# Kernel tuning notes

Measured on AMD Instinct MI355X. Metric: run time of the kernel, lower is better.

Reference implementation:

```python
import jax, jax.numpy as jnp
import numpy as np
from jax import lax

NUM_LAYERS = 3
NUM_QUBITS = 8
BATCH = 131072
DIM = 2 ** NUM_QUBITS  # 256


def _rot_mats(params):
    # params: (L, Q, 3) angles for RX, RY, RZ. Returns combined U = RZ @ RY @ RX, (L, Q, 2, 2) complex64.
    half = params * 0.5
    cx = jnp.cos(half[..., 0]).astype(jnp.complex64)
    sx = jnp.sin(half[..., 0]).astype(jnp.complex64)
    cy = jnp.cos(half[..., 1]).astype(jnp.complex64)
    sy = jnp.sin(half[..., 1]).astype(jnp.complex64)
    ezm = jnp.exp(-1j * half[..., 2]).astype(jnp.complex64)
    ezp = jnp.exp(1j * half[..., 2]).astype(jnp.complex64)
    zero = jnp.zeros_like(cx)
    RX = jnp.stack([jnp.stack([cx, -1j * sx], -1), jnp.stack([-1j * sx, cx], -1)], -2)
    RY = jnp.stack([jnp.stack([cy, -sy], -1), jnp.stack([sy, cy], -1)], -2)
    RZ = jnp.stack([jnp.stack([ezm, zero], -1), jnp.stack([zero, ezp], -1)], -2)
    return jnp.einsum('lqij,lqjk,lqkm->lqim', RZ, RY, RX)


def _apply_1q(state, U, wire):
    # state: (B, 2,2,...,2); wire w lives on axis w+1 (PennyLane wire 0 = most significant bit)
    ax = wire + 1
    return jnp.moveaxis(jnp.tensordot(U, state, axes=((1,), (ax,))), 0, ax)


def _apply_cnot(state, ctrl, tgt):
    c_ax, t_ax = ctrl + 1, tgt + 1
    s0 = lax.index_in_dim(state, 0, axis=c_ax, keepdims=True)
    s1 = lax.index_in_dim(state, 1, axis=c_ax, keepdims=True)
    s1 = jnp.flip(s1, axis=t_ax)
    return jnp.concatenate([s0, s1], axis=c_ax)


def _circuit(params, state_re, state_im):
    U = _rot_mats(params)  # (L, Q, 2, 2)
    state = (state_re + 1j * state_im).astype(jnp.complex64)
    state = state.reshape((state.shape[0],) + (2,) * NUM_QUBITS)
    for l in range(NUM_LAYERS):
        for q in range(NUM_QUBITS):
            state = _apply_1q(state, U[l, q], q)
        for q in range(NUM_QUBITS):
            state = _apply_cnot(state, q, (q + 1) % NUM_QUBITS)
    state = state.reshape(state.shape[0], DIM)
    # probability that wire 0 measures |0>: sum |amp|^2 over first half of amplitudes
    half = state[:, : DIM // 2]
    return jnp.sum(half.real ** 2 + half.imag ** 2, axis=1).astype(jnp.float32)


def setup_inputs() -> dict:
    key = jax.random.key(0)
    k1, k2, k3 = jax.random.split(key, 3)
    params = jax.random.uniform(k1, (NUM_LAYERS, NUM_QUBITS, 3), dtype=jnp.float32)
    sr = jax.random.normal(k2, (BATCH, DIM), dtype=jnp.float32)
    si = jax.random.normal(k3, (BATCH, DIM), dtype=jnp.float32)
    norm = jnp.sqrt(jnp.sum(sr ** 2 + si ** 2, axis=1, keepdims=True))
    return {"params": params, "state_re": sr / norm, "state_im": si / norm}


def reference(params, state_re, state_im):
    return _circuit(params, state_re, state_im)
```

## Files before the change

### kernel.cpp

```cpp
#include <hip/hip_runtime.h>
#include <stdint.h>

#define NLAYERS 3
#define NQ 8
#define DIM 256
#define KDIM 512
#define BM 64
#define NBLK (131072 / BM)

typedef float  f32x4  __attribute__((ext_vector_type(4)));
typedef __bf16 bf16x8 __attribute__((ext_vector_type(8)));

__device__ __forceinline__ unsigned short f2bf(float f){
    union { float f; uint32_t u; } v; v.f = f;
    uint32_t u = v.u;
    u += 0x7fffu + ((u >> 16) & 1u);
    return (unsigned short)(u >> 16);
}

__device__ __forceinline__ float2 cmul(float2 a, float2 b){
    return make_float2(a.x*b.x - a.y*b.y, a.x*b.y + a.y*b.x);
}

__device__ __forceinline__ void gload_lds16(void* lds, const void* g){
    __builtin_amdgcn_global_load_lds(
        (const __attribute__((address_space(1))) unsigned int*)g,
        (__attribute__((address_space(3))) unsigned int*)lds,
        16, 0, 0);
}

__global__ __launch_bounds__(256) void build_g_kernel(const float* __restrict__ params,
                                                      unsigned short* __restrict__ G){
    __shared__ float2 st[2][DIM];
    __shared__ float2 gm[NLAYERS*NQ][4];
    const int j = blockIdx.x;
    const int i = threadIdx.x;

    if (i < NLAYERS*NQ){
        const float* pp = params + i*3;
        float hx = 0.5f*pp[0], hy = 0.5f*pp[1], hz = 0.5f*pp[2];
        float cx = cosf(hx), sx = sinf(hx);
        float cy = cosf(hy), sy = sinf(hy);
        float cz = cosf(hz), sz = sinf(hz);
        float2 ezm = make_float2(cz, -sz), ezp = make_float2(cz, sz);
        float2 m00 = make_float2( cy*cx,  sy*sx);
        float2 m01 = make_float2(-sy*cx, -cy*sx);
        float2 m10 = make_float2( sy*cx, -cy*sx);
        float2 m11 = make_float2( cy*cx, -sy*sx);
        gm[i][0] = cmul(ezm, m00);
        gm[i][1] = cmul(ezm, m01);
        gm[i][2] = cmul(ezp, m10);
        gm[i][3] = cmul(ezp, m11);
    }

    int psrc = i;
    #pragma unroll
    for (int q = NQ-1; q >= 0; --q){
        int c  = 7 - q;
        int tb = 7 - ((q + 1) & 7);
        psrc = ((psrc >> c) & 1) ? (psrc ^ (1 << tb)) : psrc;
    }

    int cur = 0;
    st[0][i] = make_float2(i == j ? 1.0f : 0.0f, 0.0f);
    __syncthreads();

    for (int l = 0; l < NLAYERS; ++l){
        for (int q = 0; q < NQ; ++q){
            float2 U0a = gm[l*NQ+q][0], U0b = gm[l*NQ+q][1];
            float2 U1a = gm[l*NQ+q][2], U1b = gm[l*NQ+q][3];
            int p  = 7 - q;
            int bs = (i >> p) & 1;
            int i0 = i & ~(1 << p), i1 = i | (1 << p);
            float2 a0 = st[cur][i0], a1 = st[cur][i1];
            float2 ua = bs ? U1a : U0a;
            float2 ub = bs ? U1b : U0b;
            float2 r;
            r.x = ua.x*a0.x - ua.y*a0.y + ub.x*a1.x - ub.y*a1.y;
            r.y = ua.x*a0.y + ua.y*a0.x + ub.x*a1.y + ub.y*a1.x;
            st[cur ^ 1][i] = r;
            cur ^= 1;
            __syncthreads();
        }
        float2 r = st[cur][psrc];
        st[cur ^ 1][i] = r;
        cur ^= 1;
        __syncthreads();
    }

    const int m = i & 127;
    float2 a = st[cur][m];
    unsigned short lo, hi;
    if (i < 128){ lo = f2bf(a.x); hi = f2bf(-a.y); }
    else        { lo = f2bf(a.y); hi = f2bf( a.x); }
    G[(size_t)i*KDIM + j]        = lo;
    G[(size_t)i*KDIM + j + DIM]  = hi;
}

__global__ __launch_bounds__(256, 3) void qform_kernel(const float* __restrict__ sr,
                                                       const float* __restrict__ si,
                                                       const unsigned short* __restrict__ G,
                                                       float* __restrict__ out){
    __shared__ float          As[BM * 64];
    __shared__ unsigned short Bs[DIM * 64];
    __shared__ float red[4 * BM];

    const int tid  = threadIdx.x;
    const int lane = tid & 63;
    const int w    = tid >> 6;
    const int l15  = lane & 15;
    const int quad = lane >> 4;
    const int x7   = l15 & 7;
    const size_t mbase = (size_t)blockIdx.x * BM;

    f32x4 acc[4][4];
    const f32x4 vzero = {0.0f, 0.0f, 0.0f, 0.0f};
    #pragma unroll
    for (int ii = 0; ii < 4; ++ii)
        #pragma unroll
        for (int jj = 0; jj < 4; ++jj)
            acc[ii][jj] = vzero;

    for (int kc = 0; kc < 8; ++kc){
        __syncthreads();
        {
            const float* Zsrc = (kc < 4) ? sr : si;
            const int kcol = (kc & 3) * 64;
            #pragma unroll
            for (int i = 0; i < 4; ++i){
                const int c  = w*4 + i;
                const int ar = c*4 + (lane >> 4);
                const int gg = (lane & 15) ^ (ar & 7);
                const float* gp = Zsrc + (mbase + ar)*DIM + kcol + gg*4;
                gload_lds16(&As[c*256], gp);
            }
        }
        {
            #pragma unroll
            for (int i = 0; i < 8; ++i){
                const int c  = w*8 + i;
                const int rb = c*8 + (lane >> 3);
                const int gb = (lane & 7) ^ (rb & 7);
                const unsigned short* gp = G + (size_t)rb*KDIM + kc*64 + gb*8;
                gload_lds16(&Bs[c*512], gp);
            }
        }
        __syncthreads();

        #pragma unroll
        for (int ks = 0; ks < 2; ++ks){
            bf16x8 a[4], b[4];
            const int g0 = ks*8 + quad*2;
            #pragma unroll
            for (int ii = 0; ii < 4; ++ii){
                const int m = ii*16 + l15;
                union { float4 v; uint32_t u[4]; } h0, h1;
                h0.v = *(const float4*)&As[m*64 + ((g0    ) ^ x7)*4];
                h1.v = *(const float4*)&As[m*64 + ((g0 + 1) ^ x7)*4];
                union { uint32_t u[4]; bf16x8 f; } pk;
                pk.u[0] = __builtin_amdgcn_perm(h0.u[1], h0.u[0], 0x07060302);
                pk.u[1] = __builtin_amdgcn_perm(h0.u[3], h0.u[2], 0x07060302);
                pk.u[2] = __builtin_amdgcn_perm(h1.u[1], h1.u[0], 0x07060302);
                pk.u[3] = __builtin_amdgcn_perm(h1.u[3], h1.u[2], 0x07060302);
                a[ii] = pk.f;
            }
            const int gB = ks*4 + quad;
            #pragma unroll
            for (int jj = 0; jj < 4; ++jj){
                const int n = w*64 + jj*16 + l15;
                b[jj] = *(const bf16x8*)&Bs[n*64 + (gB ^ x7)*8];
            }
            #pragma unroll
            for (int ii = 0; ii < 4; ++ii)
                #pragma unroll
                for (int jj = 0; jj < 4; ++jj)
                    acc[ii][jj] = __builtin_amdgcn_mfma_f32_16x16x32_bf16(
                        a[ii], b[jj], acc[ii][jj], 0, 0, 0);
        }
    }

    float s[4][4];
    #pragma unroll
    for (int ii = 0; ii < 4; ++ii)
        #pragma unroll
        for (int r = 0; r < 4; ++r){
            float t = 0.0f;
            #pragma unroll
            for (int jj = 0; jj < 4; ++jj){ float v = acc[ii][jj][r]; t += v*v; }
            s[ii][r] = t;
        }
    #pragma unroll
    for (int ii = 0; ii < 4; ++ii)
        #pragma unroll
        for (int r = 0; r < 4; ++r){
            float t = s[ii][r];
            t += __shfl_xor(t, 1);
            t += __shfl_xor(t, 2);
            t += __shfl_xor(t, 4);
            t += __shfl_xor(t, 8);
            s[ii][r] = t;
        }
    if (l15 == 0){
        #pragma unroll
        for (int ii = 0; ii < 4; ++ii)
            #pragma unroll
            for (int r = 0; r < 4; ++r)
                red[w*64 + ii*16 + quad*4 + r] = s[ii][r];
    }
    __syncthreads();
    if (tid < 64){
        float o = red[tid] + red[64 + tid] + red[128 + tid] + red[192 + tid];
        out[mbase + tid] = o;
    }
}

extern "C" void kernel_launch(void* const* d_in, const int* in_sizes, int n_in,
                              void* d_out, int out_size, void* d_ws, size_t ws_size,
                              hipStream_t stream){
    const float* params = (const float*)d_in[0];
    const float* sr     = (const float*)d_in[1];
    const float* si     = (const float*)d_in[2];
    unsigned short* G   = (unsigned short*)d_ws;
    float* out          = (float*)d_out;

    build_g_kernel<<<dim3(DIM), dim3(256), 0, stream>>>(params, G);
    qform_kernel<<<dim3(NBLK), dim3(256), 0, stream>>>(sr, si, G, out);
}
```

Measured before the change: 289.3 us.

## Keep whole half-unitary in LDS and stream state rows directly into registers

Replaces the real-embedded 512x256 GEMM with a complex 256x128 product: the weight image (real and imaginary parts of the first half of the unitary) is loaded into LDS once per 1024-thread persistent block. State rows are then read straight from global into registers with one-step prefetch, using four MFMAs per complex tile. Only the wire-0 half of outputs is computed, which removes half the B-matrix work and avoids the per-k-chunk LDS staging and barriers. The costs are a 128KB LDS footprint that allows one block per CU, uncoalesced per-lane row loads, and serialized loops with unroll 1.

```diff
diff --git a/kernel.cpp b/kernel.cpp
--- a/kernel.cpp
+++ b/kernel.cpp
@@ -4,9 +4,8 @@
 #define NLAYERS 3
 #define NQ 8
 #define DIM 256
-#define KDIM 512
-#define BM 64
-#define NBLK (131072 / BM)
+#define HALF 128
+#define BATCH 131072
 
 typedef float  f32x4  __attribute__((ext_vector_type(4)));
 typedef __bf16 bf16x8 __attribute__((ext_vector_type(8)));
@@ -29,8 +28,8 @@
         16, 0, 0);
 }
 
-__global__ __launch_bounds__(256) void build_g_kernel(const float* __restrict__ params,
-                                                      unsigned short* __restrict__ G){
+__global__ __launch_bounds__(256) void build_w_kernel(const float* __restrict__ params,
+                                                      unsigned short* __restrict__ W){
     __shared__ float2 st[2][DIM];
     __shared__ float2 gm[NLAYERS*NQ][4];
     const int j = blockIdx.x;
@@ -90,127 +89,110 @@
 
     const int m = i & 127;
     float2 a = st[cur][m];
-    unsigned short lo, hi;
-    if (i < 128){ lo = f2bf(a.x); hi = f2bf(-a.y); }
-    else        { lo = f2bf(a.y); hi = f2bf( a.x); }
-    G[(size_t)i*KDIM + j]        = lo;
-    G[(size_t)i*KDIM + j + DIM]  = hi;
-}
-
-__global__ __launch_bounds__(256, 3) void qform_kernel(const float* __restrict__ sr,
-                                                       const float* __restrict__ si,
-                                                       const unsigned short* __restrict__ G,
-                                                       float* __restrict__ out){
-    __shared__ float          As[BM * 64];
-    __shared__ unsigned short Bs[DIM * 64];
-    __shared__ float red[4 * BM];
+    const uint32_t off = (uint32_t)m*256u
+                       + ((((uint32_t)j >> 3) ^ ((uint32_t)m & 7u)) << 3)
+                       + ((uint32_t)j & 7u);
+    if (i < 128) W[off]          = f2bf(a.x);
+    else         W[32768u + off] = f2bf(a.y);
+}
+
+__global__ __launch_bounds__(1024) void qform2_kernel(const float* __restrict__ sr,
+                                                      const float* __restrict__ si,
+                                                      const unsigned short* __restrict__ W,
+                                                      float* __restrict__ out){
+    __shared__ unsigned short Bs[65536];
 
     const int tid  = threadIdx.x;
     const int lane = tid & 63;
     const int w    = tid >> 6;
     const int l15  = lane & 15;
     const int quad = lane >> 4;
-    const int x7   = l15 & 7;
-    const size_t mbase = (size_t)blockIdx.x * BM;
-
-    f32x4 acc[4][4];
-    const f32x4 vzero = {0.0f, 0.0f, 0.0f, 0.0f};
+
     #pragma unroll
-    for (int ii = 0; ii < 4; ++ii)
+    for (int r = 0; r < 8; ++r){
+        const int c = w*8 + r;
+        gload_lds16(&Bs[c*512], W + (size_t)c*512 + lane*8);
+    }
+    __syncthreads();
+
+    const size_t row0 = (size_t)blockIdx.x * 512 + (size_t)w * 32;
+
+    #pragma unroll 1
+    for (int t = 0; t < 2; ++t){
+        const float* ar = sr + (row0 + (size_t)(t*16 + l15)) * DIM;
+        const float* ai = si + (row0 + (size_t)(t*16 + l15)) * DIM;
+
+        f32x4 accR[8], accI[8];
+        const f32x4 z = {0.0f, 0.0f, 0.0f, 0.0f};
         #pragma unroll
-        for (int jj = 0; jj < 4; ++jj)
-            acc[ii][jj] = vzero;
-
-    for (int kc = 0; kc < 8; ++kc){
-        __syncthreads();
-        {
-            const float* Zsrc = (kc < 4) ? sr : si;
-            const int kcol = (kc & 3) * 64;
+        for (int jf = 0; jf < 8; ++jf){ accR[jf] = z; accI[jf] = z; }
+
+        float4 r0 = *(const float4*)(ar + quad*8);
+        float4 r1 = *(const float4*)(ar + quad*8 + 4);
+        float4 q0 = *(const float4*)(ai + quad*8);
+        float4 q1 = *(const float4*)(ai + quad*8 + 4);
+
+        #pragma unroll 1
+        for (int ks = 0; ks < 8; ++ks){
+            union { float4 v; uint32_t u[4]; } ha, hb;
+            union { uint32_t u[4]; bf16x8 f; } pr, pi, pn;
+            ha.v = r0; hb.v = r1;
+            pr.u[0] = __builtin_amdgcn_perm(ha.u[1], ha.u[0], 0x07060302);
+            pr.u[1] = __builtin_amdgcn_perm(ha.u[3], ha.u[2], 0x07060302);
+            pr.u[2] = __builtin_amdgcn_perm(hb.u[1], hb.u[0], 0x07060302);
+            pr.u[3] = __builtin_amdgcn_perm(hb.u[3], hb.u[2], 0x07060302);
+            ha.v = q0; hb.v = q1;
+            pi.u[0] = __builtin_amdgcn_perm(ha.u[1], ha.u[0], 0x07060302);
+            pi.u[1] = __builtin_amdgcn_perm(ha.u[3], ha.u[2], 0x07060302);
+            pi.u[2] = __builtin_amdgcn_perm(hb.u[1], hb.u[0], 0x07060302);
+            pi.u[3] = __builtin_amdgcn_perm(hb.u[3], hb.u[2], 0x07060302);
+            pn.u[0] = pi.u[0] ^ 0x80008000u;
+            pn.u[1] = pi.u[1] ^ 0x80008000u;
+            pn.u[2] = pi.u[2] ^ 0x80008000u;
+            pn.u[3] = pi.u[3] ^ 0x80008000u;
+            const bf16x8 fr = pr.f;
+            const bf16x8 fi = pi.f;
+            const bf16x8 fn = pn.f;
+
+            const int nk = (ks < 7) ? (ks + 1) : 7;
+            r0 = *(const float4*)(ar + nk*32 + quad*8);
+            r1 = *(const float4*)(ar + nk*32 + quad*8 + 4);
+            q0 = *(const float4*)(ai + nk*32 + quad*8);
+            q1 = *(const float4*)(ai + nk*32 + quad*8 + 4);
+
+            const int ub = l15*256 + (((ks*4 + quad) ^ (l15 & 7)) << 3);
+
             #pragma unroll
-            for (int i = 0; i < 4; ++i){
-                const int c  = w*4 + i;
-                const int ar = c*4 + (lane >> 4);
-                const int gg = (lane & 15) ^ (ar & 7);
-                const float* gp = Zsrc + (mbase + ar)*DIM + kcol + gg*4;
-                gload_lds16(&As[c*256], gp);
+            for (int jf = 0; jf < 8; ++jf){
+                const bf16x8 br = *(const bf16x8*)&Bs[ub + jf*4096];
+                const bf16x8 bi = *(const bf16x8*)&Bs[32768 + ub + jf*4096];
+                accR[jf] = __builtin_amdgcn_mfma_f32_16x16x32_bf16(fr, br, accR[jf], 0, 0, 0);
+                accR[jf] = __builtin_amdgcn_mfma_f32_16x16x32_bf16(fn, bi, accR[jf], 0, 0, 0);
+                accI[jf] = __builtin_amdgcn_mfma_f32_16x16x32_bf16(fr, bi, accI[jf], 0, 0, 0);
+                accI[jf] = __builtin_amdgcn_mfma_f32_16x16x32_bf16(fi, br, accI[jf], 0, 0, 0);
             }
         }
-        {
-            #pragma unroll
-            for (int i = 0; i < 8; ++i){
-                const int c  = w*8 + i;
-                const int rb = c*8 + (lane >> 3);
-                const int gb = (lane & 7) ^ (rb & 7);
-                const unsigned short* gp = G + (size_t)rb*KDIM + kc*64 + gb*8;
-                gload_lds16(&Bs[c*512], gp);
-            }
-        }
-        __syncthreads();
-
-        #pragma unroll
-        for (int ks = 0; ks < 2; ++ks){
-            bf16x8 a[4], b[4];
-            const int g0 = ks*8 + quad*2;
-            #pragma unroll
-            for (int ii = 0; ii < 4; ++ii){
-                const int m = ii*16 + l15;
-                union { float4 v; uint32_t u[4]; } h0, h1;
-                h0.v = *(const float4*)&As[m*64 + ((g0    ) ^ x7)*4];
-                h1.v = *(const float4*)&As[m*64 + ((g0 + 1) ^ x7)*4];
-                union { uint32_t u[4]; bf16x8 f; } pk;
-                pk.u[0] = __builtin_amdgcn_perm(h0.u[1], h0.u[0], 0x07060302);
-                pk.u[1] = __builtin_amdgcn_perm(h0.u[3], h0.u[2], 0x07060302);
-                pk.u[2] = __builtin_amdgcn_perm(h1.u[1], h1.u[0], 0x07060302);
-                pk.u[3] = __builtin_amdgcn_perm(h1.u[3], h1.u[2], 0x07060302);
-                a[ii] = pk.f;
-            }
-            const int gB = ks*4 + quad;
-            #pragma unroll
-            for (int jj = 0; jj < 4; ++jj){
-                const int n = w*64 + jj*16 + l15;
-                b[jj] = *(const bf16x8*)&Bs[n*64 + (gB ^ x7)*8];
-            }
-            #pragma unroll
-            for (int ii = 0; ii < 4; ++ii)
-                #pragma unroll
-                for (int jj = 0; jj < 4; ++jj)
-                    acc[ii][jj] = __builtin_amdgcn_mfma_f32_16x16x32_bf16(
-                        a[ii], b[jj], acc[ii][jj], 0, 0, 0);
-        }
-    }
-
-    float s[4][4];
-    #pragma unroll
-    for (int ii = 0; ii < 4; ++ii)
+
+        float s[4];
         #pragma unroll
         for (int r = 0; r < 4; ++r){
-            float t = 0.0f;
+            float tt = 0.0f;
             #pragma unroll
-            for (int jj = 0; jj < 4; ++jj){ float v = acc[ii][jj][r]; t += v*v; }
-            s[ii][r] = t;
-        }
-    #pragma unroll
-    for (int ii = 0; ii < 4; ++ii)
-        #pragma unroll
-        for (int r = 0; r < 4; ++r){
-            float t = s[ii][r];
-            t += __shfl_xor(t, 1);
-            t += __shfl_xor(t, 2);
-            t += __shfl_xor(t, 4);
-            t += __shfl_xor(t, 8);
-            s[ii][r] = t;
-        }
-    if (l15 == 0){
-        #pragma unroll
-        for (int ii = 0; ii < 4; ++ii)
-            #pragma unroll
-            for (int r = 0; r < 4; ++r)
-                red[w*64 + ii*16 + quad*4 + r] = s[ii][r];
-    }
-    __syncthreads();
-    if (tid < 64){
-        float o = red[tid] + red[64 + tid] + red[128 + tid] + red[192 + tid];
-        out[mbase + tid] = o;
+            for (int jf = 0; jf < 8; ++jf){
+                const float vr = accR[jf][r];
+                const float vi = accI[jf][r];
+                tt += vr*vr + vi*vi;
+            }
+            tt += __shfl_xor(tt, 1);
+            tt += __shfl_xor(tt, 2);
+            tt += __shfl_xor(tt, 4);
+            tt += __shfl_xor(tt, 8);
+            s[r] = tt;
+        }
+        if (l15 == 0){
+            float4 o; o.x = s[0]; o.y = s[1]; o.z = s[2]; o.w = s[3];
+            *(float4*)(out + row0 + t*16 + quad*4) = o;
+        }
     }
 }
 
@@ -220,9 +202,9 @@
     const float* params = (const float*)d_in[0];
     const float* sr     = (const float*)d_in[1];
     const float* si     = (const float*)d_in[2];
-    unsigned short* G   = (unsigned short*)d_ws;
+    unsigned short* Wimg = (unsigned short*)d_ws;
     float* out          = (float*)d_out;
 
-    build_g_kernel<<<dim3(DIM), dim3(256), 0, stream>>>(params, G);
-    qform_kernel<<<dim3(NBLK), dim3(256), 0, stream>>>(sr, si, G, out);
-}
+    build_w_kernel<<<dim3(DIM), dim3(256), 0, stream>>>(params, Wimg);
+    qform2_kernel<<<dim3(256), dim3(1024), 0, stream>>>(sr, si, Wimg, out);
+}
```

After: 297.5 us. 2.8% more time.
